# Optimization experiments

Measured on AMD Instinct MI355X. Metric: run time of the kernel, lower is better.

Reference implementation:

```python
import jax, jax.numpy as jnp
import numpy as np

B, T, H, A = 64, 512, 1024, 300


def setup_inputs() -> dict:
    key = jax.random.key(0)
    ks = jax.random.split(key, 12)
    s = 0.02  # weight init scale
    return {
        "hidden": jax.random.normal(ks[0], (B, T, H), jnp.float32),
        "aspect": jax.random.normal(ks[1], (B, 1, A), jnp.float32),
        # torch Linear stores weight as [out_features, in_features]
        "W_h": jax.random.normal(ks[2], (H, H), jnp.float32) * s,
        "b_h": jax.random.normal(ks[3], (H,), jnp.float32) * s,
        "W_v": jax.random.normal(ks[4], (A, A), jnp.float32) * s,
        "b_v": jax.random.normal(ks[5], (A,), jnp.float32) * s,
        "w_w": jax.random.normal(ks[6], (1, H + A), jnp.float32) * s,
        "w_b": jax.random.normal(ks[7], (1,), jnp.float32) * s,
        "W_p": jax.random.normal(ks[8], (H, H), jnp.float32) * s,
        "b_p": jax.random.normal(ks[9], (H,), jnp.float32) * s,
        "W_x": jax.random.normal(ks[10], (H, H), jnp.float32) * s,
        "b_x": jax.random.normal(ks[11], (H,), jnp.float32) * s,
    }


def reference(hidden, aspect, W_h, b_h, W_v, b_v, w_w, w_b, W_p, b_p, W_x, b_x):
    # transformed aspect: [B, 1, A], repeated along seq dim -> [B, T, A]
    tv = aspect @ W_v.T + b_v
    rep_v = jnp.broadcast_to(tv, (hidden.shape[0], hidden.shape[1], tv.shape[-1]))
    # M = tanh(concat(W_h(hidden), repeated_v)) : [B, T, H+A]
    M = jnp.tanh(jnp.concatenate([hidden @ W_h.T + b_h, rep_v], axis=-1))
    # additive attention scores -> softmax over T
    scores = jnp.einsum("bts,os->bto", M, w_w)[..., 0] + w_b[0]  # [B, T]
    alpha = jax.nn.softmax(scores, axis=-1)
    # weighted sum r = alpha^T @ hidden : [B, 1, H]
    r = jnp.einsum("bt,bth->bh", alpha, hidden)[:, None, :]
    # NOTE: faithful to original torch broadcasting quirk:
    # [B,1,H] + [B,H] broadcasts to [B,B,H]
    output = jnp.tanh((r @ W_p.T + b_p) + (hidden[:, -1, :] @ W_x.T + b_x))
    return output
```

## Files before the change

### kernel.cpp

```cpp
#include <hip/hip_runtime.h>
#include <hip/hip_bf16.h>
#include <stdint.h>

#define B_DIM 64
#define T_DIM 512
#define H_DIM 1024
#define M_DIM (B_DIM * T_DIM)

typedef __bf16 bf16x8 __attribute__((ext_vector_type(8)));
typedef float f32x4 __attribute__((ext_vector_type(4)));

__device__ __forceinline__ float tanh_fast(float x) {
  float e = __expf(2.0f * x);
  return 1.0f - 2.0f / (e + 1.0f);
}

__device__ __forceinline__ float bf2f(unsigned short u) {
  return __uint_as_float(((unsigned int)u) << 16);
}

__device__ __forceinline__ void async_cp16(const void* gp, void* lp) {
  __builtin_amdgcn_global_load_lds(
      reinterpret_cast<const __attribute__((address_space(1))) uint32_t*>(
          reinterpret_cast<uintptr_t>(gp)),
      reinterpret_cast<__attribute__((address_space(3))) uint32_t*>(
          reinterpret_cast<uintptr_t>(lp)),
      16, 0, 0);
}

__global__ void cvt_kernel(const float* __restrict__ src, __bf16* __restrict__ dst, int n4) {
  int i = blockIdx.x * 256 + threadIdx.x;
  if (i >= n4) return;
  float4 v = reinterpret_cast<const float4*>(src)[i];
  union { __bf16 b[4]; uint2 u; } o;
  o.b[0] = (__bf16)v.x; o.b[1] = (__bf16)v.y; o.b[2] = (__bf16)v.z; o.b[3] = (__bf16)v.w;
  reinterpret_cast<uint2*>(dst)[i] = o.u;
}

#define GM_BK 64
__global__ __launch_bounds__(256) void gemm_scores_kernel(
    const __bf16* __restrict__ A, const __bf16* __restrict__ Bm,
    const float* __restrict__ bh, const float* __restrict__ ww,
    float* __restrict__ scores, int K) {
  __shared__ __attribute__((aligned(16))) __bf16 lA[128 * GM_BK];
  __shared__ __attribute__((aligned(16))) __bf16 lB[128 * GM_BK];

  const int tid = threadIdx.x;
  const int bid = blockIdx.x;
  const int m0 = (bid & 255) * 128;
  const int n0 = (bid >> 8) * 128;

  const int wv = tid >> 6;
  const int lane = tid & 63;
  const int wm = wv & 1, wn = wv >> 1;
  const int r16 = lane & 15, quad = lane >> 4;

  f32x4 acc[4][4] = {};

  const __bf16* gA[4]; const __bf16* gB[4];
  __bf16* lAd[4]; __bf16* lBd[4];
#pragma unroll
  for (int j = 0; j < 4; ++j) {
    int c = j * 256 + tid;
    int row = c >> 3;
    int p = c & 7;
    int kc = p ^ ((row >> 1) & 7);
    gA[j] = A + (size_t)(m0 + row) * K + kc * 8;
    gB[j] = Bm + (size_t)(n0 + row) * K + kc * 8;
    lAd[j] = &lA[c * 8];
    lBd[j] = &lB[c * 8];
  }

  const int sw = r16 >> 1;
  const __bf16* pa[2]; const __bf16* pb[2];
#pragma unroll
  for (int kk = 0; kk < 2; ++kk) {
    pa[kk] = &lA[(wm * 64 + r16) * GM_BK + ((kk * 4 + quad) ^ sw) * 8];
    pb[kk] = &lB[(wn * 64 + r16) * GM_BK + ((kk * 4 + quad) ^ sw) * 8];
  }

  for (int k0 = 0; k0 < K; k0 += GM_BK) {
#pragma unroll
    for (int j = 0; j < 4; ++j) async_cp16(gA[j] + k0, lAd[j]);
#pragma unroll
    for (int j = 0; j < 4; ++j) async_cp16(gB[j] + k0, lBd[j]);
    __syncthreads();
#pragma unroll
    for (int kk = 0; kk < 2; ++kk) {
      bf16x8 af[4], bfr[4];
#pragma unroll
      for (int i = 0; i < 4; ++i) af[i] = *reinterpret_cast<const bf16x8*>(pa[kk] + i * 16 * GM_BK);
#pragma unroll
      for (int i = 0; i < 4; ++i) bfr[i] = *reinterpret_cast<const bf16x8*>(pb[kk] + i * 16 * GM_BK);
#pragma unroll
      for (int mi = 0; mi < 4; ++mi)
#pragma unroll
        for (int ni = 0; ni < 4; ++ni)
          acc[mi][ni] = __builtin_amdgcn_mfma_f32_16x16x32_bf16(af[mi], bfr[ni], acc[mi][ni], 0, 0, 0);
    }
    __syncthreads();
  }

  float bhv[4], wwv[4];
#pragma unroll
  for (int ni = 0; ni < 4; ++ni) {
    int n = n0 + wn * 64 + ni * 16 + r16;
    bhv[ni] = bh[n];
    wwv[ni] = ww[n];
  }
#pragma unroll
  for (int mi = 0; mi < 4; ++mi) {
#pragma unroll
    for (int rg = 0; rg < 4; ++rg) {
      float s = 0.f;
#pragma unroll
      for (int ni = 0; ni < 4; ++ni)
        s += tanh_fast(acc[mi][ni][rg] + bhv[ni]) * wwv[ni];
      s += __shfl_xor(s, 1, 16);
      s += __shfl_xor(s, 2, 16);
      s += __shfl_xor(s, 4, 16);
      s += __shfl_xor(s, 8, 16);
      if (r16 == 0) {
        int m = m0 + wm * 64 + mi * 16 + quad * 4 + rg;
        atomicAdd(&scores[m], s);
      }
    }
  }
}

__global__ void softmax_kernel(const float* __restrict__ scores, float* __restrict__ alpha) {
  __shared__ float wred[4], wsum[4];
  const int b = blockIdx.x, tid = threadIdx.x;
  const int wv = tid >> 6, lane = tid & 63;
  float v0 = scores[b * T_DIM + tid];
  float v1 = scores[b * T_DIM + 256 + tid];
  float mx = fmaxf(v0, v1);
#pragma unroll
  for (int off = 1; off < 64; off <<= 1) mx = fmaxf(mx, __shfl_xor(mx, off, 64));
  if (lane == 0) wred[wv] = mx;
  __syncthreads();
  mx = fmaxf(fmaxf(wred[0], wred[1]), fmaxf(wred[2], wred[3]));
  float e0 = __expf(v0 - mx), e1 = __expf(v1 - mx);
  float s = e0 + e1;
#pragma unroll
  for (int off = 1; off < 64; off <<= 1) s += __shfl_xor(s, off, 64);
  if (lane == 0) wsum[wv] = s;
  __syncthreads();
  s = wsum[0] + wsum[1] + wsum[2] + wsum[3];
  float inv = 1.0f / s;
  alpha[b * T_DIM + tid] = e0 * inv;
  alpha[b * T_DIM + 256 + tid] = e1 * inv;
}

__global__ void weighted_sum_kernel(const __bf16* __restrict__ hiddenBf,
                                    const float* __restrict__ alpha,
                                    float* __restrict__ r) {
  __shared__ float al[64];
  const int b = blockIdx.y, tc = blockIdx.x, tid = threadIdx.x;
  if (tid < 64) al[tid] = alpha[b * T_DIM + tc * 64 + tid];
  __syncthreads();
  const __bf16* hp = hiddenBf + (size_t)b * T_DIM * H_DIM + (size_t)tc * 64 * H_DIM + tid * 4;
  float4 acc = make_float4(0.f, 0.f, 0.f, 0.f);
#pragma unroll 8
  for (int t = 0; t < 64; ++t) {
    float a = al[t];
    ushort4 u = *reinterpret_cast<const ushort4*>(hp + (size_t)t * H_DIM);
    acc.x += a * bf2f(u.x);
    acc.y += a * bf2f(u.y);
    acc.z += a * bf2f(u.z);
    acc.w += a * bf2f(u.w);
  }
  float* rp = r + b * H_DIM + tid * 4;
  atomicAdd(rp + 0, acc.x);
  atomicAdd(rp + 1, acc.y);
  atomicAdd(rp + 2, acc.z);
  atomicAdd(rp + 3, acc.w);
}

__global__ void rowvec_matT_kernel(const float* __restrict__ src, size_t src_stride,
                                   const float* __restrict__ W, const float* __restrict__ bias,
                                   float* __restrict__ dst) {
  __shared__ float sv[H_DIM];
  const int i = blockIdx.y, h0 = blockIdx.x * 64, tid = threadIdx.x;
  reinterpret_cast<float4*>(sv)[tid] =
      reinterpret_cast<const float4*>(src + (size_t)i * src_stride)[tid];
  __syncthreads();
  const int hl = tid >> 2;
  const int kq = tid & 3;
  const float* wr = W + (size_t)(h0 + hl) * H_DIM + kq * 256;
  const float* svp = sv + kq * 256;
  float acc = 0.f;
#pragma unroll 4
  for (int k = 0; k < 256; k += 4) {
    float4 w4 = *reinterpret_cast<const float4*>(wr + k);
    float4 s4 = *reinterpret_cast<const float4*>(svp + k);
    acc += w4.x * s4.x + w4.y * s4.y + w4.z * s4.z + w4.w * s4.w;
  }
  acc += __shfl_xor(acc, 1, 4);
  acc += __shfl_xor(acc, 2, 4);
  if (kq == 0) dst[(size_t)i * H_DIM + h0 + hl] = acc + bias[h0 + hl];
}

__global__ void final_kernel(const float* __restrict__ rp, const float* __restrict__ xq,
                             float* __restrict__ out) {
  int idx = blockIdx.x * 256 + threadIdx.x;
  int e = idx * 4;
  int i = e >> 16;
  int j = (e >> 10) & 63;
  int h = e & 1023;
  float4 a = *reinterpret_cast<const float4*>(&rp[i * H_DIM + h]);
  float4 b = *reinterpret_cast<const float4*>(&xq[j * H_DIM + h]);
  float4 o;
  o.x = tanh_fast(a.x + b.x);
  o.y = tanh_fast(a.y + b.y);
  o.z = tanh_fast(a.z + b.z);
  o.w = tanh_fast(a.w + b.w);
  *reinterpret_cast<float4*>(&out[e]) = o;
}

extern "C" void kernel_launch(void* const* d_in, const int* in_sizes, int n_in,
                              void* d_out, int out_size, void* d_ws, size_t ws_size,
                              hipStream_t stream) {
  const float* hidden = (const float*)d_in[0];
  const float* W_h = (const float*)d_in[2];
  const float* b_h = (const float*)d_in[3];
  const float* w_w = (const float*)d_in[6];
  const float* W_p = (const float*)d_in[8];
  const float* b_p = (const float*)d_in[9];
  const float* W_x = (const float*)d_in[10];
  const float* b_x = (const float*)d_in[11];
  float* out = (float*)d_out;

  char* ws = (char*)d_ws;
  __bf16* hidBf = (__bf16*)ws;
  __bf16* whBf = (__bf16*)(ws + 67108864);
  float* scores = (float*)(ws + 69206016);
  float* alpha = (float*)(ws + 69337088);
  float* r = (float*)(ws + 69468160);
  float* rp = (float*)(ws + 69730304);
  float* xq = (float*)(ws + 69992448);

  cvt_kernel<<<(M_DIM * H_DIM / 4) / 256, 256, 0, stream>>>(hidden, hidBf, M_DIM * H_DIM / 4);
  cvt_kernel<<<(H_DIM * H_DIM / 4) / 256, 256, 0, stream>>>(W_h, whBf, H_DIM * H_DIM / 4);

  hipMemsetAsync(scores, 0, M_DIM * sizeof(float), stream);
  hipMemsetAsync(r, 0, B_DIM * H_DIM * sizeof(float), stream);
  gemm_scores_kernel<<<2048, 256, 0, stream>>>(hidBf, whBf, b_h, w_w, scores, H_DIM);

  softmax_kernel<<<B_DIM, 256, 0, stream>>>(scores, alpha);

  weighted_sum_kernel<<<dim3(8, B_DIM), 256, 0, stream>>>(hidBf, alpha, r);

  rowvec_matT_kernel<<<dim3(H_DIM / 64, B_DIM), 256, 0, stream>>>(r, (size_t)H_DIM, W_p, b_p, rp);
  rowvec_matT_kernel<<<dim3(H_DIM / 64, B_DIM), 256, 0, stream>>>(
      hidden + (size_t)(T_DIM - 1) * H_DIM, (size_t)T_DIM * H_DIM, W_x, b_x, xq);

  final_kernel<<<(B_DIM * B_DIM * H_DIM / 4) / 256, 256, 0, stream>>>(rp, xq, out);
}
```

Measured before the change: 419.9 us.

## Enlarge GEMM M-tile to 256 and fuse softmax into weighted sum

The scores GEMM tile grows from 128x128 to 256x128, so each wave computes an 8x4 MFMA grid, the K loop is fully unrolled and launch bounds request 2 blocks per CU. This raises the reuse of each loaded B tile and halves the number of blocks. Separately, the weight conversion and zeroing of scores and r are merged into one kernel, replacing a cvt launch and two memsets, and the softmax is recomputed inside each weighted-sum block so the alpha buffer and its kernel go away. Costs are higher register and LDS use per block, fewer blocks in flight, and softmax statistics recomputed redundantly in eight blocks per batch row.

```diff
diff --git a/kernel.cpp b/kernel.cpp
--- a/kernel.cpp
+++ b/kernel.cpp
@@ -5,6 +5,7 @@
 #define B_DIM 64
 #define T_DIM 512
 #define H_DIM 1024
+#define K_DIM 1024
 #define M_DIM (B_DIM * T_DIM)
 
 typedef __bf16 bf16x8 __attribute__((ext_vector_type(8)));
@@ -28,46 +29,70 @@
       16, 0, 0);
 }
 
-__global__ void cvt_kernel(const float* __restrict__ src, __bf16* __restrict__ dst, int n4) {
+__global__ void cvt_hidden_kernel(const float* __restrict__ src, __bf16* __restrict__ dst) {
   int i = blockIdx.x * 256 + threadIdx.x;
-  if (i >= n4) return;
   float4 v = reinterpret_cast<const float4*>(src)[i];
   union { __bf16 b[4]; uint2 u; } o;
   o.b[0] = (__bf16)v.x; o.b[1] = (__bf16)v.y; o.b[2] = (__bf16)v.z; o.b[3] = (__bf16)v.w;
   reinterpret_cast<uint2*>(dst)[i] = o.u;
 }
 
+__global__ void cvtW_zero_kernel(const float* __restrict__ Wh, __bf16* __restrict__ whBf,
+                                 float* __restrict__ scores, float* __restrict__ r) {
+  int bid = blockIdx.x, tid = threadIdx.x;
+  if (bid < 1024) {
+    int i = bid * 256 + tid;
+    float4 v = reinterpret_cast<const float4*>(Wh)[i];
+    union { __bf16 b[4]; uint2 u; } o;
+    o.b[0] = (__bf16)v.x; o.b[1] = (__bf16)v.y; o.b[2] = (__bf16)v.z; o.b[3] = (__bf16)v.w;
+    reinterpret_cast<uint2*>(whBf)[i] = o.u;
+  } else if (bid < 1056) {
+    int i = (bid - 1024) * 256 + tid;
+    reinterpret_cast<float4*>(scores)[i] = make_float4(0.f, 0.f, 0.f, 0.f);
+  } else {
+    int i = (bid - 1056) * 256 + tid;
+    reinterpret_cast<float4*>(r)[i] = make_float4(0.f, 0.f, 0.f, 0.f);
+  }
+}
+
 #define GM_BK 64
-__global__ __launch_bounds__(256) void gemm_scores_kernel(
+__global__ __launch_bounds__(256, 2) void gemm_scores_kernel(
     const __bf16* __restrict__ A, const __bf16* __restrict__ Bm,
     const float* __restrict__ bh, const float* __restrict__ ww,
-    float* __restrict__ scores, int K) {
-  __shared__ __attribute__((aligned(16))) __bf16 lA[128 * GM_BK];
+    float* __restrict__ scores) {
+  __shared__ __attribute__((aligned(16))) __bf16 lA[256 * GM_BK];
   __shared__ __attribute__((aligned(16))) __bf16 lB[128 * GM_BK];
 
   const int tid = threadIdx.x;
   const int bid = blockIdx.x;
-  const int m0 = (bid & 255) * 128;
-  const int n0 = (bid >> 8) * 128;
+  const int m0 = (bid & 127) * 256;
+  const int n0 = (bid >> 7) * 128;
 
   const int wv = tid >> 6;
   const int lane = tid & 63;
   const int wm = wv & 1, wn = wv >> 1;
   const int r16 = lane & 15, quad = lane >> 4;
 
-  f32x4 acc[4][4] = {};
-
-  const __bf16* gA[4]; const __bf16* gB[4];
-  __bf16* lAd[4]; __bf16* lBd[4];
+  f32x4 acc[8][4] = {};
+
+  const __bf16* gA[8]; __bf16* lAd[8];
+#pragma unroll
+  for (int j = 0; j < 8; ++j) {
+    int c = j * 256 + tid;
+    int row = c >> 3;
+    int p = c & 7;
+    int kc = p ^ ((row >> 1) & 7);
+    gA[j] = A + (size_t)(m0 + row) * K_DIM + kc * 8;
+    lAd[j] = &lA[c * 8];
+  }
+  const __bf16* gB[4]; __bf16* lBd[4];
 #pragma unroll
   for (int j = 0; j < 4; ++j) {
     int c = j * 256 + tid;
     int row = c >> 3;
     int p = c & 7;
     int kc = p ^ ((row >> 1) & 7);
-    gA[j] = A + (size_t)(m0 + row) * K + kc * 8;
-    gB[j] = Bm + (size_t)(n0 + row) * K + kc * 8;
-    lAd[j] = &lA[c * 8];
+    gB[j] = Bm + (size_t)(n0 + row) * K_DIM + kc * 8;
     lBd[j] = &lB[c * 8];
   }
 
@@ -75,25 +100,29 @@
   const __bf16* pa[2]; const __bf16* pb[2];
 #pragma unroll
   for (int kk = 0; kk < 2; ++kk) {
-    pa[kk] = &lA[(wm * 64 + r16) * GM_BK + ((kk * 4 + quad) ^ sw) * 8];
+    pa[kk] = &lA[(wm * 128 + r16) * GM_BK + ((kk * 4 + quad) ^ sw) * 8];
     pb[kk] = &lB[(wn * 64 + r16) * GM_BK + ((kk * 4 + quad) ^ sw) * 8];
   }
 
-  for (int k0 = 0; k0 < K; k0 += GM_BK) {
-#pragma unroll
-    for (int j = 0; j < 4; ++j) async_cp16(gA[j] + k0, lAd[j]);
+#pragma unroll
+  for (int k0 = 0; k0 < K_DIM; k0 += GM_BK) {
+#pragma unroll
+    for (int j = 0; j < 8; ++j) async_cp16(gA[j] + k0, lAd[j]);
 #pragma unroll
     for (int j = 0; j < 4; ++j) async_cp16(gB[j] + k0, lBd[j]);
     __syncthreads();
 #pragma unroll
     for (int kk = 0; kk < 2; ++kk) {
-      bf16x8 af[4], bfr[4];
-#pragma unroll
-      for (int i = 0; i < 4; ++i) af[i] = *reinterpret_cast<const bf16x8*>(pa[kk] + i * 16 * GM_BK);
-#pragma unroll
-      for (int i = 0; i < 4; ++i) bfr[i] = *reinterpret_cast<const bf16x8*>(pb[kk] + i * 16 * GM_BK);
-#pragma unroll
-      for (int mi = 0; mi < 4; ++mi)
+      bf16x8 bfr[4];
+#pragma unroll
+      for (int ni = 0; ni < 4; ++ni)
+        bfr[ni] = *reinterpret_cast<const bf16x8*>(pb[kk] + ni * 16 * GM_BK);
+      bf16x8 af[8];
+#pragma unroll
+      for (int mi = 0; mi < 8; ++mi)
+        af[mi] = *reinterpret_cast<const bf16x8*>(pa[kk] + mi * 16 * GM_BK);
+#pragma unroll
+      for (int mi = 0; mi < 8; ++mi)
 #pragma unroll
         for (int ni = 0; ni < 4; ++ni)
           acc[mi][ni] = __builtin_amdgcn_mfma_f32_16x16x32_bf16(af[mi], bfr[ni], acc[mi][ni], 0, 0, 0);
@@ -109,7 +138,7 @@
     wwv[ni] = ww[n];
   }
 #pragma unroll
-  for (int mi = 0; mi < 4; ++mi) {
+  for (int mi = 0; mi < 8; ++mi) {
 #pragma unroll
     for (int rg = 0; rg < 4; ++rg) {
       float s = 0.f;
@@ -121,43 +150,37 @@
       s += __shfl_xor(s, 4, 16);
       s += __shfl_xor(s, 8, 16);
       if (r16 == 0) {
-        int m = m0 + wm * 64 + mi * 16 + quad * 4 + rg;
+        int m = m0 + wm * 128 + mi * 16 + quad * 4 + rg;
         atomicAdd(&scores[m], s);
       }
     }
   }
 }
 
-__global__ void softmax_kernel(const float* __restrict__ scores, float* __restrict__ alpha) {
-  __shared__ float wred[4], wsum[4];
-  const int b = blockIdx.x, tid = threadIdx.x;
+__global__ void wsum_kernel(const float* __restrict__ scores,
+                            const __bf16* __restrict__ hiddenBf,
+                            float* __restrict__ r) {
+  __shared__ float al[64];
+  __shared__ float red[8];
+  const int bid = blockIdx.x, tid = threadIdx.x;
+  const int b = bid >> 3, tc = bid & 7;
   const int wv = tid >> 6, lane = tid & 63;
   float v0 = scores[b * T_DIM + tid];
   float v1 = scores[b * T_DIM + 256 + tid];
   float mx = fmaxf(v0, v1);
 #pragma unroll
   for (int off = 1; off < 64; off <<= 1) mx = fmaxf(mx, __shfl_xor(mx, off, 64));
-  if (lane == 0) wred[wv] = mx;
-  __syncthreads();
-  mx = fmaxf(fmaxf(wred[0], wred[1]), fmaxf(wred[2], wred[3]));
+  if (lane == 0) red[wv] = mx;
+  __syncthreads();
+  mx = fmaxf(fmaxf(red[0], red[1]), fmaxf(red[2], red[3]));
   float e0 = __expf(v0 - mx), e1 = __expf(v1 - mx);
   float s = e0 + e1;
 #pragma unroll
   for (int off = 1; off < 64; off <<= 1) s += __shfl_xor(s, off, 64);
-  if (lane == 0) wsum[wv] = s;
-  __syncthreads();
-  s = wsum[0] + wsum[1] + wsum[2] + wsum[3];
-  float inv = 1.0f / s;
-  alpha[b * T_DIM + tid] = e0 * inv;
-  alpha[b * T_DIM + 256 + tid] = e1 * inv;
-}
-
-__global__ void weighted_sum_kernel(const __bf16* __restrict__ hiddenBf,
-                                    const float* __restrict__ alpha,
-                                    float* __restrict__ r) {
-  __shared__ float al[64];
-  const int b = blockIdx.y, tc = blockIdx.x, tid = threadIdx.x;
-  if (tid < 64) al[tid] = alpha[b * T_DIM + tc * 64 + tid];
+  if (lane == 0) red[4 + wv] = s;
+  __syncthreads();
+  float inv = 1.0f / (red[4] + red[5] + red[6] + red[7]);
+  if (tid < 64) al[tid] = __expf(scores[b * T_DIM + tc * 64 + tid] - mx) * inv;
   __syncthreads();
   const __bf16* hp = hiddenBf + (size_t)b * T_DIM * H_DIM + (size_t)tc * 64 * H_DIM + tid * 4;
   float4 acc = make_float4(0.f, 0.f, 0.f, 0.f);
@@ -235,21 +258,16 @@
   __bf16* hidBf = (__bf16*)ws;
   __bf16* whBf = (__bf16*)(ws + 67108864);
   float* scores = (float*)(ws + 69206016);
-  float* alpha = (float*)(ws + 69337088);
   float* r = (float*)(ws + 69468160);
   float* rp = (float*)(ws + 69730304);
   float* xq = (float*)(ws + 69992448);
 
-  cvt_kernel<<<(M_DIM * H_DIM / 4) / 256, 256, 0, stream>>>(hidden, hidBf, M_DIM * H_DIM / 4);
-  cvt_kernel<<<(H_DIM * H_DIM / 4) / 256, 256, 0, stream>>>(W_h, whBf, H_DIM * H_DIM / 4);
-
-  hipMemsetAsync(scores, 0, M_DIM * sizeof(float), stream);
-  hipMemsetAsync(r, 0, B_DIM * H_DIM * sizeof(float), stream);
-  gemm_scores_kernel<<<2048, 256, 0, stream>>>(hidBf, whBf, b_h, w_w, scores, H_DIM);
-
-  softmax_kernel<<<B_DIM, 256, 0, stream>>>(scores, alpha);
-
-  weighted_sum_kernel<<<dim3(8, B_DIM), 256, 0, stream>>>(hidBf, alpha, r);
+  cvt_hidden_kernel<<<M_DIM * H_DIM / 1024, 256, 0, stream>>>(hidden, hidBf);
+  cvtW_zero_kernel<<<1072, 256, 0, stream>>>(W_h, whBf, scores, r);
+
+  gemm_scores_kernel<<<1024, 256, 0, stream>>>(hidBf, whBf, b_h, w_w, scores);
+
+  wsum_kernel<<<512, 256, 0, stream>>>(scores, hidBf, r);
 
   rowvec_matT_kernel<<<dim3(H_DIM / 64, B_DIM), 256, 0, stream>>>(r, (size_t)H_DIM, W_p, b_p, rp);
   rowvec_matT_kernel<<<dim3(H_DIM / 64, B_DIM), 256, 0, stream>>>(
```

After: 383.6 us. 8.6% less time.
